# Kernel optimization log

Hardware: AMD Instinct MI355X
Metric: run time of the kernel (lower is better)

The kernel has to match this reference:

```python
import jax, jax.numpy as jnp
import numpy as np


def setup_inputs() -> dict:
    key = jax.random.key(0)
    B, H, C, T = 8, 8, 64, 2048
    qkv = jax.random.normal(key, (B, 3 * H * C, T), dtype=jnp.float32)
    return {"qkv": qkv, "n_heads": H}


def reference(qkv, n_heads):
    # qkv: (B, 3*H*C, T)
    bs, width, length = qkv.shape
    ch = width // (3 * n_heads)
    q, k, v = jnp.split(qkv, 3, axis=1)          # each (B, H*C, T)
    scale = ch ** (-0.25)
    q = (q * scale).reshape(bs * n_heads, ch, length)
    k = (k * scale).reshape(bs * n_heads, ch, length)
    v = v.reshape(bs * n_heads, ch, length)
    # weight[b, t, s] = sum_c q[b,c,t] * k[b,c,s]
    weight = jnp.einsum('bct,bcs->bts', q, k)
    weight = jax.nn.softmax(weight.astype(jnp.float32), axis=-1).astype(qkv.dtype)
    out = jnp.einsum('bts,bcs->bct', weight, v)   # (B*H, C, T)
    return out.reshape(bs, n_heads * ch, length)
```

## Files before the change

kernel.cpp:

```cpp
#include <hip/hip_runtime.h>

typedef __bf16 bf16x4 __attribute__((ext_vector_type(4)));
typedef __bf16 bf16x8 __attribute__((ext_vector_type(8)));
typedef float floatx4 __attribute__((ext_vector_type(4)));
typedef float floatx16 __attribute__((ext_vector_type(16)));

#define T_SEQ 2048
#define TTILE 512
#define STILE 64
#define LOG2E_SCALE 0.18033688011112042f

__device__ __forceinline__ unsigned pack_bf16_pair(float a, float b) {
    unsigned ua = __builtin_bit_cast(unsigned, a) + 0x8000u;
    unsigned ub = __builtin_bit_cast(unsigned, b) + 0x8000u;
    return __builtin_amdgcn_perm(ub, ua, 0x07060302u);
}
__device__ __forceinline__ unsigned short bf16_bits(float a) {
    return (unsigned short)((__builtin_bit_cast(unsigned, a) + 0x8000u) >> 16);
}

__global__ __launch_bounds__(512, 2) void attn_fused(
    const float* __restrict__ qkv, float* __restrict__ out)
{
    __shared__ __align__(16) __bf16 Kt[2][STILE][72];
    __shared__ __align__(16) __bf16 Vs[2][64][72];

    const int tid  = threadIdx.x;
    const int lane = tid & 63;
    const int wave = tid >> 6;
    const int l31  = lane & 31;
    const int g    = lane >> 5;

    const int bh = blockIdx.y;
    const int b = bh >> 3, head = bh & 7;
    const size_t in_base = ((size_t)b * 1536 + head * 64) * T_SEQ;
    const float* Qg = qkv + in_base;
    const float* Kg = qkv + in_base + (size_t)512 * T_SEQ;
    const float* Vg = qkv + in_base + (size_t)1024 * T_SEQ;

    const int tcol0 = blockIdx.x * TTILE + wave * 64 + l31;
    const int tcol1 = tcol0 + 32;

    bf16x8 qf[2][4];
    #pragma unroll
    for (int kb = 0; kb < 4; ++kb)
        #pragma unroll
        for (int j = 0; j < 8; ++j) {
            size_t rowoff = (size_t)(kb * 16 + g * 8 + j) * T_SEQ;
            qf[0][kb][j] = (__bf16)(Qg[rowoff + tcol0] * LOG2E_SCALE);
            qf[1][kb][j] = (__bf16)(Qg[rowoff + tcol1] * LOG2E_SCALE);
        }

    floatx16 zf;
    #pragma unroll
    for (int r = 0; r < 16; ++r) zf[r] = 0.0f;

    union U4 { unsigned u[4]; bf16x8 v; };
    U4 one0, one1;
    {
        unsigned p0 = (l31 == 0) ? 0x3F803F80u : 0u;
        unsigned p1 = (l31 == 1) ? 0x3F803F80u : 0u;
        one0.u[0] = p0; one0.u[1] = p0; one0.u[2] = p0; one0.u[3] = p0;
        one1.u[0] = p1; one1.u[1] = p1; one1.u[2] = p1; one1.u[3] = p1;
    }

    floatx16 Oa[2][2];
    floatx16 La = zf;
    Oa[0][0] = zf; Oa[0][1] = zf; Oa[1][0] = zf; Oa[1][1] = zf;

    int cc[2], ss[2];
    size_t goff[2];
    #pragma unroll
    for (int r = 0; r < 2; ++r) {
        int i = tid + r * 512;
        cc[r] = i >> 4;
        ss[r] = (i & 15) * 4;
        goff[r] = (size_t)cc[r] * T_SEQ + ss[r];
    }
    const int ph = (tid >> 1) & 3;

    floatx4 kr[2], vr[2];
    #pragma unroll
    for (int r = 0; r < 2; ++r) {
        kr[r] = *(const floatx4*)(Kg + goff[r]);
        vr[r] = *(const floatx4*)(Vg + goff[r]);
    }
    #pragma unroll
    for (int r = 0; r < 2; ++r) {
        int c = cc[r], s4 = ss[r];
        #pragma unroll
        for (int k = 0; k < 4; ++k) {
            int d = (k + ph) & 3;
            *(unsigned short*)&Kt[0][s4 + d][c] = bf16_bits(kr[r][d]);
        }
        union { unsigned u[2]; bf16x4 v; } vb;
        vb.u[0] = pack_bf16_pair(vr[r][0], vr[r][1]);
        vb.u[1] = pack_bf16_pair(vr[r][2], vr[r][3]);
        *(bf16x4*)&Vs[0][c][s4] = vb.v;
    }

    for (int it = 0; it < T_SEQ / STILE; ++it) {
        const int rb = it & 1;
        const int s_next = (it + 1) * STILE;
        const bool pref = (s_next < T_SEQ);

        __syncthreads();

        if (pref) {
            #pragma unroll
            for (int r = 0; r < 2; ++r) {
                kr[r] = *(const floatx4*)(Kg + goff[r] + s_next);
                vr[r] = *(const floatx4*)(Vg + goff[r] + s_next);
            }
        }

        const __bf16 (*KtR)[72] = Kt[rb];
        const __bf16 (*VsR)[72] = Vs[rb];

        bf16x8 pf[2][4];
        #pragma unroll
        for (int ms = 0; ms < 2; ++ms) {
            floatx16 Sa0, Sa1;
            {
                bf16x8 kf = *(const bf16x8*)&KtR[ms * 32 + l31][g * 8];
                Sa0 = __builtin_amdgcn_mfma_f32_32x32x16_bf16(kf, qf[0][0], zf, 0, 0, 0);
                Sa1 = __builtin_amdgcn_mfma_f32_32x32x16_bf16(kf, qf[1][0], zf, 0, 0, 0);
            }
            #pragma unroll
            for (int kb = 1; kb < 4; ++kb) {
                bf16x8 kf = *(const bf16x8*)&KtR[ms * 32 + l31][kb * 16 + g * 8];
                Sa0 = __builtin_amdgcn_mfma_f32_32x32x16_bf16(kf, qf[0][kb], Sa0, 0, 0, 0);
                Sa1 = __builtin_amdgcn_mfma_f32_32x32x16_bf16(kf, qf[1][kb], Sa1, 0, 0, 0);
            }
            #pragma unroll
            for (int tt = 0; tt < 2; ++tt) {
                const floatx16& Sa = tt ? Sa1 : Sa0;
                float p[16];
                #pragma unroll
                for (int r = 0; r < 16; ++r)
                    p[r] = __builtin_amdgcn_exp2f(Sa[r]);
                unsigned d[8];
                #pragma unroll
                for (int q = 0; q < 8; ++q) d[q] = pack_bf16_pair(p[2 * q], p[2 * q + 1]);
                #pragma unroll
                for (int kb = 0; kb < 2; ++kb) {
                    unsigned d0 = d[4 * kb + 0], d1 = d[4 * kb + 1];
                    unsigned d2 = d[4 * kb + 2], d3 = d[4 * kb + 3];
                    unsigned sendA = g ? d0 : d2;
                    unsigned sendB = g ? d1 : d3;
                    unsigned recvA = (unsigned)__shfl_xor((int)sendA, 32);
                    unsigned recvB = (unsigned)__shfl_xor((int)sendB, 32);
                    union { unsigned u[4]; bf16x8 v; } fu;
                    fu.u[0] = g ? recvA : d0;
                    fu.u[1] = g ? recvB : d1;
                    fu.u[2] = g ? d2    : recvA;
                    fu.u[3] = g ? d3    : recvB;
                    pf[tt][ms * 2 + kb] = fu.v;
                }
            }
        }

        #pragma unroll
        for (int mc = 0; mc < 2; ++mc)
            #pragma unroll
            for (int kb2 = 0; kb2 < 4; ++kb2) {
                bf16x8 vf = *(const bf16x8*)&VsR[mc * 32 + l31][kb2 * 16 + g * 8];
                Oa[0][mc] = __builtin_amdgcn_mfma_f32_32x32x16_bf16(vf, pf[0][kb2], Oa[0][mc], 0, 0, 0);
                Oa[1][mc] = __builtin_amdgcn_mfma_f32_32x32x16_bf16(vf, pf[1][kb2], Oa[1][mc], 0, 0, 0);
            }
        #pragma unroll
        for (int kb2 = 0; kb2 < 4; ++kb2) {
            La = __builtin_amdgcn_mfma_f32_32x32x16_bf16(one0.v, pf[0][kb2], La, 0, 0, 0);
            La = __builtin_amdgcn_mfma_f32_32x32x16_bf16(one1.v, pf[1][kb2], La, 0, 0, 0);
        }

        if (pref) {
            __bf16 (*KtW)[72] = Kt[rb ^ 1];
            __bf16 (*VsW)[72] = Vs[rb ^ 1];
            #pragma unroll
            for (int r = 0; r < 2; ++r) {
                int c = cc[r], s4 = ss[r];
                #pragma unroll
                for (int k = 0; k < 4; ++k) {
                    int d = (k + ph) & 3;
                    *(unsigned short*)&KtW[s4 + d][c] = bf16_bits(kr[r][d]);
                }
                union { unsigned u[2]; bf16x4 v; } vb;
                vb.u[0] = pack_bf16_pair(vr[r][0], vr[r][1]);
                vb.u[1] = pack_bf16_pair(vr[r][2], vr[r][3]);
                *(bf16x4*)&VsW[c][s4] = vb.v;
            }
        }
    }

    float d0 = La[0], d1 = La[1];
    float rl0 = 1.0f / (d0 + __shfl_xor(d0, 32));
    float rl1 = 1.0f / (d1 + __shfl_xor(d1, 32));

    const size_t out_base = ((size_t)b * 512 + head * 64) * T_SEQ;
    #pragma unroll
    for (int mc = 0; mc < 2; ++mc)
        #pragma unroll
        for (int r = 0; r < 16; ++r) {
            int c = mc * 32 + (r & 3) + 8 * (r >> 2) + 4 * g;
            size_t row = out_base + (size_t)c * T_SEQ;
            out[row + tcol0] = Oa[0][mc][r] * rl0;
            out[row + tcol1] = Oa[1][mc][r] * rl1;
        }
}

extern "C" void kernel_launch(void* const* d_in, const int* in_sizes, int n_in,
                              void* d_out, int out_size, void* d_ws, size_t ws_size,
                              hipStream_t stream) {
    const float* qkv = (const float*)d_in[0];
    float* out = (float*)d_out;
    dim3 grid(T_SEQ / TTILE, 64);
    attn_fused<<<grid, dim3(512), 0, stream>>>(qkv, out);
}
```

Baseline: 209.0 us.

## Permute V columns in LDS to drop P cross-lane shuffles and interleave PV MFMAs

The V tile is now stored in shared memory with its key columns permuted (bits 2 and 3 of the column index swapped), so the P fragments produced by the exp step already match the MFMA B-operand layout and the __shfl_xor exchanges between half-waves are no longer needed. The PV and row-sum MFMAs now run inside each 32-key sub-block right after its exponentials rather than after both sub-blocks, which shrinks the live P registers and lets exp work overlap with MFMAs. The risk is the correctness of the permutation mapping and possible bank conflicts on the new V store pattern.

```diff
diff --git a/kernel.cpp b/kernel.cpp
--- a/kernel.cpp
+++ b/kernel.cpp
@@ -68,13 +68,14 @@
     floatx16 La = zf;
     Oa[0][0] = zf; Oa[0][1] = zf; Oa[1][0] = zf; Oa[1][1] = zf;
 
-    int cc[2], ss[2];
+    int cc[2], ss[2], ksw[2];
     size_t goff[2];
     #pragma unroll
     for (int r = 0; r < 2; ++r) {
         int i = tid + r * 512;
         cc[r] = i >> 4;
         ss[r] = (i & 15) * 4;
+        ksw[r] = (ss[r] & ~12) | ((ss[r] & 4) << 1) | ((ss[r] & 8) >> 1);
         goff[r] = (size_t)cc[r] * T_SEQ + ss[r];
     }
     const int ph = (tid >> 1) & 3;
@@ -96,7 +97,7 @@
         union { unsigned u[2]; bf16x4 v; } vb;
         vb.u[0] = pack_bf16_pair(vr[r][0], vr[r][1]);
         vb.u[1] = pack_bf16_pair(vr[r][2], vr[r][3]);
-        *(bf16x4*)&Vs[0][c][s4] = vb.v;
+        *(bf16x4*)&Vs[0][c][ksw[r]] = vb.v;
     }
 
     for (int it = 0; it < T_SEQ / STILE; ++it) {
@@ -117,7 +118,6 @@
         const __bf16 (*KtR)[72] = Kt[rb];
         const __bf16 (*VsR)[72] = Vs[rb];
 
-        bf16x8 pf[2][4];
         #pragma unroll
         for (int ms = 0; ms < 2; ++ms) {
             floatx16 Sa0, Sa1;
@@ -132,6 +132,7 @@
                 Sa0 = __builtin_amdgcn_mfma_f32_32x32x16_bf16(kf, qf[0][kb], Sa0, 0, 0, 0);
                 Sa1 = __builtin_amdgcn_mfma_f32_32x32x16_bf16(kf, qf[1][kb], Sa1, 0, 0, 0);
             }
+            bf16x8 pf[2][2];
             #pragma unroll
             for (int tt = 0; tt < 2; ++tt) {
                 const floatx16& Sa = tt ? Sa1 : Sa0;
@@ -139,39 +140,27 @@
                 #pragma unroll
                 for (int r = 0; r < 16; ++r)
                     p[r] = __builtin_amdgcn_exp2f(Sa[r]);
-                unsigned d[8];
-                #pragma unroll
-                for (int q = 0; q < 8; ++q) d[q] = pack_bf16_pair(p[2 * q], p[2 * q + 1]);
                 #pragma unroll
                 for (int kb = 0; kb < 2; ++kb) {
-                    unsigned d0 = d[4 * kb + 0], d1 = d[4 * kb + 1];
-                    unsigned d2 = d[4 * kb + 2], d3 = d[4 * kb + 3];
-                    unsigned sendA = g ? d0 : d2;
-                    unsigned sendB = g ? d1 : d3;
-                    unsigned recvA = (unsigned)__shfl_xor((int)sendA, 32);
-                    unsigned recvB = (unsigned)__shfl_xor((int)sendB, 32);
                     union { unsigned u[4]; bf16x8 v; } fu;
-                    fu.u[0] = g ? recvA : d0;
-                    fu.u[1] = g ? recvB : d1;
-                    fu.u[2] = g ? d2    : recvA;
-                    fu.u[3] = g ? d3    : recvB;
-                    pf[tt][ms * 2 + kb] = fu.v;
+                    #pragma unroll
+                    for (int d = 0; d < 4; ++d)
+                        fu.u[d] = pack_bf16_pair(p[8 * kb + 2 * d], p[8 * kb + 2 * d + 1]);
+                    pf[tt][kb] = fu.v;
                 }
             }
-        }
-
-        #pragma unroll
-        for (int mc = 0; mc < 2; ++mc)
-            #pragma unroll
-            for (int kb2 = 0; kb2 < 4; ++kb2) {
-                bf16x8 vf = *(const bf16x8*)&VsR[mc * 32 + l31][kb2 * 16 + g * 8];
-                Oa[0][mc] = __builtin_amdgcn_mfma_f32_32x32x16_bf16(vf, pf[0][kb2], Oa[0][mc], 0, 0, 0);
-                Oa[1][mc] = __builtin_amdgcn_mfma_f32_32x32x16_bf16(vf, pf[1][kb2], Oa[1][mc], 0, 0, 0);
-            }
-        #pragma unroll
-        for (int kb2 = 0; kb2 < 4; ++kb2) {
-            La = __builtin_amdgcn_mfma_f32_32x32x16_bf16(one0.v, pf[0][kb2], La, 0, 0, 0);
-            La = __builtin_amdgcn_mfma_f32_32x32x16_bf16(one1.v, pf[1][kb2], La, 0, 0, 0);
+            #pragma unroll
+            for (int kb = 0; kb < 2; ++kb) {
+                const int kb2 = ms * 2 + kb;
+                #pragma unroll
+                for (int mc = 0; mc < 2; ++mc) {
+                    bf16x8 vf = *(const bf16x8*)&VsR[mc * 32 + l31][kb2 * 16 + g * 8];
+                    Oa[0][mc] = __builtin_amdgcn_mfma_f32_32x32x16_bf16(vf, pf[0][kb], Oa[0][mc], 0, 0, 0);
+                    Oa[1][mc] = __builtin_amdgcn_mfma_f32_32x32x16_bf16(vf, pf[1][kb], Oa[1][mc], 0, 0, 0);
+                }
+                La = __builtin_amdgcn_mfma_f32_32x32x16_bf16(one0.v, pf[0][kb], La, 0, 0, 0);
+                La = __builtin_amdgcn_mfma_f32_32x32x16_bf16(one1.v, pf[1][kb], La, 0, 0, 0);
+            }
         }
 
         if (pref) {
@@ -188,7 +177,7 @@
                 union { unsigned u[2]; bf16x4 v; } vb;
                 vb.u[0] = pack_bf16_pair(vr[r][0], vr[r][1]);
                 vb.u[1] = pack_bf16_pair(vr[r][2], vr[r][3]);
-                *(bf16x4*)&VsW[c][s4] = vb.v;
+                *(bf16x4*)&VsW[c][ksw[r]] = vb.v;
             }
         }
     }
```

After: 242.5 us. +16.0%, slower.
